# Optimization experiments

Hardware: AMD Instinct MI355X
Metric: run time of the kernel (lower is better)

## Reference

```python
import jax, jax.numpy as jnp
import numpy as np

N, E, H, ED, NF, NG = 75000, 150000, 44, 10, 15000, 1500


def _seg_mean(v, idx, n):
    s = jax.ops.segment_sum(v, idx, num_segments=n)
    c = jax.ops.segment_sum(jnp.ones((v.shape[0], 1), v.dtype), idx, num_segments=n)
    return s / jnp.maximum(c, 1.0)


def setup_inputs() -> dict:
    key = jax.random.key(0)
    ks = jax.random.split(key, 26)
    p = lambda k, shape: (jax.random.normal(k, shape, dtype=jnp.float32) * 0.1)
    x = jax.random.normal(ks[0], (N, H), dtype=jnp.float32)
    edge_index = jax.random.randint(ks[1], (2, E), 0, N)
    edge_attr = jax.random.normal(ks[2], (E, ED), dtype=jnp.float32)
    node2frag = (jnp.arange(N) * NF) // N          # sorted, covers all fragments
    frag2graph = (jnp.arange(NF) * NG) // NF       # sorted, covers all graphs
    noise = jax.random.normal(ks[3], (NF, H), dtype=jnp.float32)
    return {
        "x": x, "edge_attr": edge_attr, "noise": noise,
        "W0": p(ks[4], (H, H)), "b0": jnp.zeros((H,)),
        "We1": p(ks[5], (ED, ED)), "be1": jnp.zeros((ED,)),
        "We2": p(ks[6], (ED, H * H)), "be2": jnp.zeros((H * H,)),
        "root": p(ks[7], (H, H)), "conv_b": jnp.zeros((H,)),
        "Wm": p(ks[8], (2 * H, H)), "bm": jnp.zeros((H,)),
        "Wc1": p(ks[9], (H, H)), "bc1": jnp.zeros((H,)),
        "bn_g": jnp.ones((H,)), "bn_b": jnp.zeros((H,)),
        "Wc2": p(ks[10], (H, 1)), "bc2": jnp.zeros((1,)),
        "Wp1": p(ks[11], (H, 256)), "bp1": jnp.zeros((256,)),
        "Wp2": p(ks[12], (256, 128)), "bp2": jnp.zeros((128,)),
        "Wp3": p(ks[13], (128, 1)), "bp3": jnp.zeros((1,)),
        "edge_index": edge_index, "node2frag": node2frag, "frag2graph": frag2graph,
        "n_frags": NF, "n_graphs": NG,
    }


def reference(x, edge_attr, noise, W0, b0, We1, be1, We2, be2, root, conv_b, Wm, bm,
              Wc1, bc1, bn_g, bn_b, Wc2, bc2, Wp1, bp1, Wp2, bp2, Wp3, bp3,
              edge_index, node2frag, frag2graph, n_frags, n_graphs):
    n, h = x.shape
    init = x
    out = jax.nn.relu(x @ W0 + b0)
    # edge-conditioned weight matrices (computed once; edge_attr is fixed)
    ew = (jax.nn.relu(edge_attr @ We1 + be1) @ We2 + be2).reshape(-1, h, h)  # [E,h,h]
    src, dst = edge_index[0], edge_index[1]
    for _ in range(3):  # num_step_message_passing
        msg = jnp.einsum('eh,eho->eo', out[src], ew)               # per-edge matvec
        agg = jax.ops.segment_sum(msg, dst, num_segments=n)        # aggr='add'
        m = jax.nn.relu(agg + out @ root + conv_b)                 # NNConv + relu
        out = jnp.concatenate([m, out], axis=1) @ Wm + bm          # message_layer
    nodef = out + init
    # F.normalize(dim=1)
    nodef = nodef / jnp.maximum(jnp.linalg.norm(nodef, axis=1, keepdims=True), 1e-12)
    frag = _seg_mean(nodef, node2frag, n_frags)                    # global_mean_pool
    # compressor: Linear -> BatchNorm(train stats) -> ReLU -> Linear -> Sigmoid
    z = frag @ Wc1 + bc1
    z = (z - z.mean(0)) / jnp.sqrt(z.var(0) + 1e-5) * bn_g + bn_b
    w = jax.nn.sigmoid(jax.nn.relu(z) @ Wc2 + bc2).squeeze(-1)     # [NF]
    lp = w[:, None]
    ln = 1.0 - lp
    preserve_rate = (w > 0.5).astype(jnp.float32).mean()
    static = jax.lax.stop_gradient(frag)
    cnt = jax.ops.segment_sum(jnp.ones((n_frags,), jnp.float32), frag2graph, num_segments=n_graphs)[:, None]
    gsum = jax.ops.segment_sum(static, frag2graph, num_segments=n_graphs)
    gmean = gsum / jnp.maximum(cnt, 1.0)
    gsq = jax.ops.segment_sum(static * static, frag2graph, num_segments=n_graphs)
    gvar = (gsq - cnt * gmean * gmean) / jnp.maximum(cnt - 1.0, 1.0)  # unbiased (scatter_std)
    gstd = jnp.sqrt(jnp.maximum(gvar, 0.0))
    mean_f = gmean[frag2graph]
    std_f = gstd[frag2graph]
    nmean = lp * frag + ln * mean_f
    nstd = ln * std_f
    noisy = nmean + noise * nstd
    sub = _seg_mean(noisy, frag2graph, n_graphs)
    pred = jax.nn.sigmoid(jax.nn.relu(jax.nn.relu(sub @ Wp1 + bp1) @ Wp2 + bp2) @ Wp3 + bp3)
    eps = 1e-7
    kl = 0.5 * jax.ops.segment_sum((nstd ** 2 / (std_f + eps) ** 2).mean(axis=1), frag2graph, num_segments=n_graphs)[:, None] \
         + jax.ops.segment_sum(((nmean - mean_f) / (std_f + eps)) ** 2, frag2graph, num_segments=n_graphs)
    return pred, kl.mean(), preserve_rate
```

## Files before the change

### kernel.cpp

```cpp
#include <hip/hip_runtime.h>
#include <math.h>

#define NN 75000
#define NE 150000
#define H 44
#define HS 48
#define EDIM 10
#define NFRAG 15000
#define NGRAPH 1500

typedef const float* __restrict__ cfp;
typedef float* __restrict__ fpt;
typedef const int* __restrict__ cip;
typedef int* __restrict__ ipt;

__device__ __forceinline__ float relu_(float v){ return v>0.f?v:0.f; }
__device__ __forceinline__ float sigmoid_(float v){ return 1.f/(1.f+expf(-v)); }

__global__ __launch_bounds__(256) void k_hist(cip ei, ipt cnt){
    int e = blockIdx.x*256 + threadIdx.x;
    if(e>=NE) return;
    atomicAdd(&cnt[ei[NE+e]], 1);
}

__global__ __launch_bounds__(1024) void k_scan1(cip cnt, ipt incl, ipt bsum){
    __shared__ int sd[1024];
    int i = blockIdx.x*1024 + threadIdx.x;
    int v = (i<NN)? cnt[i] : 0;
    sd[threadIdx.x]=v;
    __syncthreads();
    for(int off=1; off<1024; off<<=1){
        int t = (threadIdx.x>=off)? sd[threadIdx.x-off] : 0;
        __syncthreads();
        sd[threadIdx.x]+=t;
        __syncthreads();
    }
    if(i<NN) incl[i]=sd[threadIdx.x];
    if(threadIdx.x==1023) bsum[blockIdx.x]=sd[1023];
}

__global__ void k_scan2(ipt bsum, int nblk){
    if(threadIdx.x==0 && blockIdx.x==0){
        int run=0;
        for(int b=0;b<nblk;b++){ int t=bsum[b]; bsum[b]=run; run+=t; }
    }
}

__global__ __launch_bounds__(1024) void k_scan3(cip incl, cip bsum, ipt rowptr){
    int i = blockIdx.x*1024 + threadIdx.x;
    if(i==0) rowptr[0]=0;
    if(i<NN) rowptr[i+1] = incl[i] + bsum[i>>10];
}

__global__ __launch_bounds__(256) void k_scatter(cip ei, cip rowptr, ipt cur, ipt eidx){
    int e = blockIdx.x*256 + threadIdx.x;
    if(e>=NE) return;
    int d = ei[NE+e];
    int pos = rowptr[d] + atomicAdd(&cur[d],1);
    eidx[pos]=e;
}

__global__ __launch_bounds__(256) void k_in(cfp x, cfp W0, cfp b0, fpt out){
    __shared__ float sW[H*H];
    __shared__ float sb[H];
    for(int i=threadIdx.x;i<H*H;i+=256) sW[i]=W0[i];
    if(threadIdx.x<H) sb[threadIdx.x]=b0[threadIdx.x];
    __syncthreads();
    int n = blockIdx.x*256 + threadIdx.x;
    if(n>=NN) return;
    float xv[H];
    const float4* xp = (const float4*)(x + (size_t)n*H);
    #pragma unroll
    for(int i=0;i<11;i++){ float4 v=xp[i]; xv[4*i]=v.x; xv[4*i+1]=v.y; xv[4*i+2]=v.z; xv[4*i+3]=v.w; }
    float acc[H];
    #pragma unroll
    for(int o=0;o<H;o++) acc[o]=sb[o];
    #pragma unroll
    for(int h=0;h<H;h++){
        float xh = xv[h];
        const float4* wr = (const float4*)(sW + h*H);
        #pragma unroll
        for(int o=0;o<11;o++){
            float4 w = wr[o];
            acc[4*o]+=xh*w.x; acc[4*o+1]+=xh*w.y; acc[4*o+2]+=xh*w.z; acc[4*o+3]+=xh*w.w;
        }
    }
    #pragma unroll
    for(int o=0;o<H;o++) acc[o]=relu_(acc[o]);
    float* row = out + (size_t)n*HS;
    #pragma unroll
    for(int s=0;s<4;s++){
        float4* p=(float4*)(row + s*12);
        p[0]=make_float4(acc[11*s+0],acc[11*s+1],acc[11*s+2],acc[11*s+3]);
        p[1]=make_float4(acc[11*s+4],acc[11*s+5],acc[11*s+6],acc[11*s+7]);
        p[2]=make_float4(acc[11*s+8],acc[11*s+9],acc[11*s+10],0.f);
    }
}

#define NB2 256
__global__ __launch_bounds__(256,3) void k_b2(cfp out, cfp be2, fpt b2){
    __shared__ float ovT[HS*NB2];
    int tid=threadIdx.x, lane=tid&63;
    int og = __builtin_amdgcn_readfirstlane(tid>>6);
    size_t base=(size_t)blockIdx.x*NB2;
    { size_t n=base+tid; size_t nc = n<NN? n : NN-1;
      const float4* orow=(const float4*)(out + nc*HS);
      #pragma unroll
      for(int i=0;i<12;i++){ float4 v=orow[i];
        ovT[(4*i+0)*NB2+tid]=v.x; ovT[(4*i+1)*NB2+tid]=v.y;
        ovT[(4*i+2)*NB2+tid]=v.z; ovT[(4*i+3)*NB2+tid]=v.w; }
    }
    __syncthreads();
    float m[4][11];
    #pragma unroll
    for(int j=0;j<4;j++)
        #pragma unroll
        for(int o=0;o<11;o++) m[j][o]=0.f;
    const float* wog = be2 + og*11;
    #pragma unroll
    for(int h=0;h<H;h++){
        int hl = h + h/11;
        const float4* ovp=(const float4*)(ovT + hl*NB2 + lane*4);
        float4 ov=ovp[0];
        #pragma unroll
        for(int o=0;o<11;o++){
            float w = wog[h*H+o];
            m[0][o]+=ov.x*w; m[1][o]+=ov.y*w; m[2][o]+=ov.z*w; m[3][o]+=ov.w*w;
        }
    }
    size_t n0 = base + (size_t)lane*4;
    #pragma unroll
    for(int j=0;j<4;j++){
        size_t n=n0+j;
        if(n<NN){
            float4* p=(float4*)(b2 + n*HS + og*12);
            p[0]=make_float4(m[j][0],m[j][1],m[j][2],m[j][3]);
            p[1]=make_float4(m[j][4],m[j][5],m[j][6],m[j][7]);
            p[2]=make_float4(m[j][8],m[j][9],m[j][10],0.f);
        }
    }
}

__global__ __launch_bounds__(256) void k_edge(cfp ea, cfp We1, cfp be1, fpt t){
    __shared__ float sW[EDIM*EDIM];
    __shared__ float sb[EDIM];
    if(threadIdx.x<EDIM*EDIM) sW[threadIdx.x]=We1[threadIdx.x];
    if(threadIdx.x<EDIM) sb[threadIdx.x]=be1[threadIdx.x];
    __syncthreads();
    int e = blockIdx.x*256 + threadIdx.x;
    if(e>=NE) return;
    float acc[EDIM];
    #pragma unroll
    for(int j=0;j<EDIM;j++) acc[j]=sb[j];
    #pragma unroll
    for(int k=0;k<EDIM;k++){
        float a = ea[(size_t)e*EDIM + k];
        #pragma unroll
        for(int j=0;j<EDIM;j++) acc[j]+=a*sW[k*EDIM+j];
    }
    #pragma unroll
    for(int j=0;j<EDIM;j++) t[(size_t)e*EDIM+j]=relu_(acc[j]);
}

#define EBM 256
__global__ __launch_bounds__(256,2) void k_msg(cfp out, cfp b2, cfp t, cfp We2, cip ei, fpt msg){
    __shared__ float ovT[HS*EBM];
    __shared__ float tT[EDIM*EBM];
    int tid=threadIdx.x, lane=tid&63;
    int og = __builtin_amdgcn_readfirstlane(tid>>6);
    size_t base=(size_t)blockIdx.x*EBM;
    { size_t e=base+tid; size_t ec = e<NE? e : NE-1;
      int s = ei[ec];
      const float4* orow=(const float4*)(out + (size_t)s*HS);
      #pragma unroll
      for(int i=0;i<12;i++){ float4 v=orow[i];
        ovT[(4*i+0)*EBM+tid]=v.x; ovT[(4*i+1)*EBM+tid]=v.y;
        ovT[(4*i+2)*EBM+tid]=v.z; ovT[(4*i+3)*EBM+tid]=v.w; }
      const float2* trow=(const float2*)(t + ec*EDIM);
      #pragma unroll
      for(int i=0;i<5;i++){ float2 v=trow[i]; tT[(2*i+0)*EBM+tid]=v.x; tT[(2*i+1)*EBM+tid]=v.y; }
    }
    __syncthreads();
    size_t e0 = base + (size_t)lane*4;
    int srcj[4];
    #pragma unroll
    for(int j=0;j<4;j++){ size_t e=e0+j; srcj[j]=ei[e<NE? e : NE-1]; }
    float m[4][11];
    #pragma unroll
    for(int j=0;j<4;j++){
        const float4* br=(const float4*)(b2 + (size_t)srcj[j]*HS + og*12);
        float4 A=br[0],B=br[1],C=br[2];
        m[j][0]=A.x; m[j][1]=A.y; m[j][2]=A.z; m[j][3]=A.w;
        m[j][4]=B.x; m[j][5]=B.y; m[j][6]=B.z; m[j][7]=B.w;
        m[j][8]=C.x; m[j][9]=C.y; m[j][10]=C.z;
    }
    const float* wog = We2 + og*11;
    for(int k=0;k<EDIM;k++){
        const float4* tp=(const float4*)(tT + k*EBM + lane*4);
        float4 t4=tp[0];
        const float* wk = wog + k*(H*H);
        #pragma unroll
        for(int h=0;h<H;h++){
            int hl = h + h/11;
            const float4* ovp=(const float4*)(ovT + hl*EBM + lane*4);
            float4 ov=ovp[0];
            float z0=t4.x*ov.x, z1=t4.y*ov.y, z2=t4.z*ov.z, z3=t4.w*ov.w;
            #pragma unroll
            for(int o=0;o<11;o++){
                float w = wk[h*H+o];
                m[0][o]+=z0*w; m[1][o]+=z1*w; m[2][o]+=z2*w; m[3][o]+=z3*w;
            }
        }
    }
    #pragma unroll
    for(int j=0;j<4;j++){
        size_t e=e0+j;
        if(e<NE){
            float4* p=(float4*)(msg + e*HS + og*12);
            p[0]=make_float4(m[j][0],m[j][1],m[j][2],m[j][3]);
            p[1]=make_float4(m[j][4],m[j][5],m[j][6],m[j][7]);
            p[2]=make_float4(m[j][8],m[j][9],m[j][10],0.f);
        }
    }
}

#define NBC 128
__global__ __launch_bounds__(256,3) void k_comb(cfp out, cfp msg, cip rowptr, cip eidx,
                                                cfp root, cfp conv_b, cfp Wm, cfp bm, fpt out_nxt){
    __shared__ float ovT[HS*NBC];
    __shared__ float mT[HS*NBC];
    int tid=threadIdx.x, lane=tid&63;
    int og = __builtin_amdgcn_readfirstlane(tid>>6);
    size_t base=(size_t)blockIdx.x*NBC;
    { int nl=tid>>1, half=tid&1;
      size_t n=base+nl; size_t nc = n<NN? n : NN-1;
      const float4* orow=(const float4*)(out + nc*HS + half*24);
      #pragma unroll
      for(int i=0;i<6;i++){ float4 v=orow[i];
        ovT[(half*24+4*i+0)*NBC+nl]=v.x; ovT[(half*24+4*i+1)*NBC+nl]=v.y;
        ovT[(half*24+4*i+2)*NBC+nl]=v.z; ovT[(half*24+4*i+3)*NBC+nl]=v.w; }
    }
    __syncthreads();
    size_t n0 = base + (size_t)lane*2;
    float m[2][11];
    #pragma unroll
    for(int j=0;j<2;j++)
        #pragma unroll
        for(int o=0;o<11;o++) m[j][o]=conv_b[og*11+o];
    #pragma unroll
    for(int j=0;j<2;j++){
        size_t n=n0+j; size_t nc = n<NN? n : NN-1;
        int st=rowptr[nc], en=rowptr[nc+1];
        for(int idx=st; idx<en; idx++){
            int e=eidx[idx];
            const float4* p=(const float4*)(msg + (size_t)e*HS + og*12);
            float4 A=p[0],B=p[1],C=p[2];
            m[j][0]+=A.x; m[j][1]+=A.y; m[j][2]+=A.z; m[j][3]+=A.w;
            m[j][4]+=B.x; m[j][5]+=B.y; m[j][6]+=B.z; m[j][7]+=B.w;
            m[j][8]+=C.x; m[j][9]+=C.y; m[j][10]+=C.z;
        }
    }
    const float* rog = root + og*11;
    #pragma unroll
    for(int h=0;h<H;h++){
        int hl = h + h/11;
        const float2* ovp=(const float2*)(ovT + hl*NBC + lane*2);
        float2 ov=ovp[0];
        #pragma unroll
        for(int o=0;o<11;o++){
            float w = rog[h*H+o];
            m[0][o]+=ov.x*w; m[1][o]+=ov.y*w;
        }
    }
    #pragma unroll
    for(int j=0;j<2;j++)
        #pragma unroll
        for(int o=0;o<11;o++) m[j][o]=relu_(m[j][o]);
    #pragma unroll
    for(int j=0;j<2;j++)
        #pragma unroll
        for(int o=0;o<11;o++) mT[(og*12+o)*NBC + lane*2+j]=m[j][o];
    __syncthreads();
    float no[2][11];
    #pragma unroll
    for(int j=0;j<2;j++)
        #pragma unroll
        for(int o=0;o<11;o++) no[j][o]=bm[og*11+o];
    const float* wmog = Wm + og*11;
    #pragma unroll
    for(int h=0;h<H;h++){
        int hl = h + h/11;
        const float2* mp=(const float2*)(mT + hl*NBC + lane*2);
        const float2* ovp=(const float2*)(ovT + hl*NBC + lane*2);
        float2 mh=mp[0], ov=ovp[0];
        #pragma unroll
        for(int o=0;o<11;o++){
            float a = wmog[h*H+o];
            float b = wmog[(H+h)*H+o];
            no[0][o]+=mh.x*a+ov.x*b;
            no[1][o]+=mh.y*a+ov.y*b;
        }
    }
    #pragma unroll
    for(int j=0;j<2;j++){
        size_t n=n0+j;
        if(n<NN){
            float4* p=(float4*)(out_nxt + n*HS + og*12);
            p[0]=make_float4(no[j][0],no[j][1],no[j][2],no[j][3]);
            p[1]=make_float4(no[j][4],no[j][5],no[j][6],no[j][7]);
            p[2]=make_float4(no[j][8],no[j][9],no[j][10],0.f);
        }
    }
}

__global__ __launch_bounds__(256,2) void k_frag(cfp out, cfp x, cfp Wc1, cfp bc1,
                                                fpt frag, fpt z, fpt colstat){
    __shared__ float nd[250*45];
    __shared__ float frS[50*45];
    __shared__ float sW[H*H];
    int tid=threadIdx.x;
    for(int i=tid;i<H*H;i+=256) sW[i]=Wc1[i];
    if(tid<250){
        int n = blockIdx.x*250 + tid;
        float v[H];
        const float4* xp=(const float4*)(x + (size_t)n*H);
        #pragma unroll
        for(int i=0;i<11;i++){ float4 a=xp[i]; v[4*i]=a.x; v[4*i+1]=a.y; v[4*i+2]=a.z; v[4*i+3]=a.w; }
        const float4* orow=(const float4*)(out + (size_t)n*HS);
        #pragma unroll
        for(int s=0;s<4;s++){
            float4 A=orow[3*s+0],B=orow[3*s+1],C=orow[3*s+2];
            v[11*s+0]+=A.x; v[11*s+1]+=A.y; v[11*s+2]+=A.z; v[11*s+3]+=A.w;
            v[11*s+4]+=B.x; v[11*s+5]+=B.y; v[11*s+6]+=B.z; v[11*s+7]+=B.w;
            v[11*s+8]+=C.x; v[11*s+9]+=C.y; v[11*s+10]+=C.z;
        }
        float ss=0.f;
        #pragma unroll
        for(int o=0;o<H;o++) ss+=v[o]*v[o];
        float inv = 1.f/fmaxf(sqrtf(ss),1e-12f);
        #pragma unroll
        for(int o=0;o<H;o++) nd[tid*45+o]=v[o]*inv;
    }
    __syncthreads();
    if(tid<50){
        float fr[H];
        #pragma unroll
        for(int o=0;o<H;o++) fr[o]=0.f;
        for(int j=0;j<5;j++){
            int r=tid*5+j;
            #pragma unroll
            for(int o=0;o<H;o++) fr[o]+=nd[r*45+o];
        }
        #pragma unroll
        for(int o=0;o<H;o++){ fr[o]*=0.2f; frS[tid*45+o]=fr[o]; }
        int f = blockIdx.x*50 + tid;
        float4* fw=(float4*)(frag + (size_t)f*H);
        #pragma unroll
        for(int i=0;i<11;i++) fw[i]=make_float4(fr[4*i],fr[4*i+1],fr[4*i+2],fr[4*i+3]);
    }
    __syncthreads();
    int fl=tid>>2, q=tid&3;
    int flc = fl<50? fl : 0;
    bool fv = fl<50;
    float zr[11];
    #pragma unroll
    for(int o=0;o<11;o++) zr[o]=bc1[q*11+o];
    for(int h=0;h<H;h++){
        float fh = frS[flc*45+h];
        #pragma unroll
        for(int o=0;o<11;o++) zr[o]+=fh*sW[h*H+q*11+o];
    }
    #pragma unroll
    for(int o=0;o<11;o++) if(!fv) zr[o]=0.f;
    if(fv){
        int f = blockIdx.x*50 + fl;
        #pragma unroll
        for(int o=0;o<11;o++) z[(size_t)f*H + q*11+o]=zr[o];
    }
    #pragma unroll
    for(int o=0;o<11;o++){
        float s=zr[o], sq=zr[o]*zr[o];
        #pragma unroll
        for(int d=4;d<64;d<<=1){ s+=__shfl_xor(s,d); sq+=__shfl_xor(sq,d); }
        if((tid&63)<4){
            atomicAdd(colstat + q*11+o, s);
            atomicAdd(colstat + H + q*11+o, sq);
        }
    }
}

__global__ __launch_bounds__(256) void k_bnw(cfp z, cfp colstat, cfp bng, cfp bnb, cfp Wc2, cfp bc2, fpt w, fpt pres){
    int f = blockIdx.x*256 + threadIdx.x;
    bool valid = f < NFRAG;
    int fc = valid ? f : NFRAG-1;
    float s = 0.f;
    #pragma unroll
    for(int o=0;o<H;o++){
        float mean = colstat[o]*(1.f/NFRAG);
        float var  = colstat[H+o]*(1.f/NFRAG) - mean*mean;
        float zb = (z[(size_t)fc*H+o]-mean)*rsqrtf(var+1e-5f)*bng[o]+bnb[o];
        s += relu_(zb)*Wc2[o];
    }
    float wv = sigmoid_(s + bc2[0]);
    if(valid) w[f]=wv;
    unsigned long long msk = __ballot(valid && (wv > 0.5f));
    if((threadIdx.x&63)==0) atomicAdd(pres,(float)__popcll(msk));
}

__global__ __launch_bounds__(64) void k_graph(cfp frag, cfp w, cfp noise, fpt sub, fpt klg){
    int g = blockIdx.x;
    int o = threadIdx.x;
    bool act = o < H;
    int oc = act ? o : 0;
    float frv[10];
    #pragma unroll
    for(int j=0;j<10;j++) frv[j] = act ? frag[(size_t)(10*g+j)*H + oc] : 0.f;
    float gs=0.f, gq=0.f;
    #pragma unroll
    for(int j=0;j<10;j++){ gs+=frv[j]; gq+=frv[j]*frv[j]; }
    float gmean = gs*0.1f;
    float gvar  = (gq - 10.f*gmean*gmean)*(1.f/9.f);
    float gstd  = sqrtf(fmaxf(gvar,0.f));
    float se    = gstd + 1e-7f;
    float c     = act ? (gstd/se)*(gstd/se) : 0.f;
    float C = c;
    #pragma unroll
    for(int dlt=32;dlt>0;dlt>>=1) C+=__shfl_xor(C,dlt);
    float subacc=0.f, B=0.f, Sln=0.f;
    #pragma unroll
    for(int j=0;j<10;j++){
        float lp = w[10*g+j];
        float ln = 1.f-lp;
        Sln += ln*ln;
        float nm = lp*frv[j] + ln*gmean;
        float ns = ln*gstd;
        float ny = nm + (act ? noise[(size_t)(10*g+j)*H + oc] : 0.f)*ns;
        subacc += ny;
        float dd = (nm-gmean)/se;
        B += dd*dd;
    }
    if(act) sub[(size_t)g*H+o] = subacc*0.1f;
    float Bv = act ? B : 0.f;
    #pragma unroll
    for(int dlt=32;dlt>0;dlt>>=1) Bv+=__shfl_xor(Bv,dlt);
    if(o==0) klg[g] = 0.5f*C*Sln + Bv;
}

__global__ __launch_bounds__(256) void k_pred(cfp sub, cfp Wp1, cfp bp1, cfp Wp2, cfp bp2,
                                              cfp Wp3, cfp bp3, fpt outp){
    __shared__ float ssub[H];
    __shared__ float sh1[256];
    __shared__ float sh2[128];
    int g = blockIdx.x; int tid = threadIdx.x;
    if(tid<H) ssub[tid] = sub[(size_t)g*H+tid];
    __syncthreads();
    float a = bp1[tid];
    for(int o=0;o<H;o++) a += ssub[o]*Wp1[(size_t)o*256+tid];
    sh1[tid]=relu_(a);
    __syncthreads();
    if(tid<128){
        float b = bp2[tid];
        for(int i=0;i<256;i++) b += sh1[i]*Wp2[(size_t)i*128+tid];
        sh2[tid]=relu_(b);
    }
    __syncthreads();
    if(tid<64){
        float s = sh2[tid]*Wp3[tid] + sh2[tid+64]*Wp3[tid+64];
        #pragma unroll
        for(int dlt=32;dlt>0;dlt>>=1) s+=__shfl_xor(s,dlt);
        if(tid==0) outp[g]=sigmoid_(s+bp3[0]);
    }
}

__global__ void k_final(cfp klg, cfp pres, fpt outp){
    float s = 0.f;
    for(int i=threadIdx.x;i<NGRAPH;i+=256) s+=klg[i];
    __shared__ float red[4];
    #pragma unroll
    for(int dlt=32;dlt>0;dlt>>=1) s+=__shfl_xor(s,dlt);
    int wid = threadIdx.x>>6;
    if((threadIdx.x&63)==0) red[wid]=s;
    __syncthreads();
    if(threadIdx.x==0){
        float tot = red[0]+red[1]+red[2]+red[3];
        outp[NGRAPH]   = tot/(float)(NGRAPH*H);
        outp[NGRAPH+1] = pres[0]/(float)NFRAG;
    }
}

extern "C" void kernel_launch(void* const* d_in, const int* in_sizes, int n_in,
                              void* d_out, int out_size, void* d_ws, size_t ws_size,
                              hipStream_t stream) {
    (void)in_sizes; (void)n_in; (void)out_size; (void)ws_size;
    const float* x        =(const float*)d_in[0];
    const float* edge_attr=(const float*)d_in[1];
    const float* noise    =(const float*)d_in[2];
    const float* W0       =(const float*)d_in[3];
    const float* b0       =(const float*)d_in[4];
    const float* We1      =(const float*)d_in[5];
    const float* be1      =(const float*)d_in[6];
    const float* We2      =(const float*)d_in[7];
    const float* be2      =(const float*)d_in[8];
    const float* root     =(const float*)d_in[9];
    const float* conv_b   =(const float*)d_in[10];
    const float* Wm       =(const float*)d_in[11];
    const float* bm       =(const float*)d_in[12];
    const float* Wc1      =(const float*)d_in[13];
    const float* bc1      =(const float*)d_in[14];
    const float* bng      =(const float*)d_in[15];
    const float* bnb      =(const float*)d_in[16];
    const float* Wc2      =(const float*)d_in[17];
    const float* bc2      =(const float*)d_in[18];
    const float* Wp1      =(const float*)d_in[19];
    const float* bp1      =(const float*)d_in[20];
    const float* Wp2      =(const float*)d_in[21];
    const float* bp2      =(const float*)d_in[22];
    const float* Wp3      =(const float*)d_in[23];
    const float* bp3      =(const float*)d_in[24];
    const int*   ei       =(const int*)d_in[25];

    float* ws = (float*)d_ws;
    const size_t NHS = (size_t)NN*HS;
    float* out_a  = ws;
    float* out_b  = out_a + NHS;
    float* b2_a   = out_b + NHS;
    float* b2_b   = b2_a + NHS;
    float* tbuf   = b2_b + NHS;
    float* msgbuf = tbuf + (size_t)NE*EDIM;
    float* frag   = msgbuf + (size_t)NE*HS;
    float* zbuf   = frag + (size_t)NFRAG*H;
    float* wv     = zbuf + (size_t)NFRAG*H;
    float* sub    = wv + NFRAG;
    float* klg    = sub + (size_t)NGRAPH*H;
    int*   rowptr = (int*)(klg + NGRAPH);
    int*   eidx   = rowptr + (NN+1);
    int*   bsum   = eidx + NE;
    int*   incl   = bsum + 128;
    int*   cnt    = incl + NN;
    int*   cur    = cnt + NN;
    float* colstat= (float*)(cur + NN);
    float* pres   = colstat + 2*H;

    hipMemsetAsync(cnt, 0, (size_t)(2*NN + 2*H + 8)*sizeof(float), stream);

    const int nb_n  = (NN + 255)/256;
    const int nb_e  = (NE + 255)/256;
    const int nb_f  = (NFRAG + 255)/256;
    const int nblk  = (NN + 1023)/1024;
    const int nb_c  = (NN + NBC-1)/NBC;

    k_hist   <<<nb_e,256,0,stream>>>(ei, cnt);
    k_scan1  <<<nblk,1024,0,stream>>>(cnt, incl, bsum);
    k_scan2  <<<1,64,0,stream>>>(bsum, nblk);
    k_scan3  <<<nblk,1024,0,stream>>>(incl, bsum, rowptr);
    k_scatter<<<nb_e,256,0,stream>>>(ei, rowptr, cur, eidx);

    k_in  <<<nb_n,256,0,stream>>>(x, W0, b0, out_a);
    k_b2  <<<nb_n,256,0,stream>>>(out_a, be2, b2_a);
    k_edge<<<nb_e,256,0,stream>>>(edge_attr, We1, be1, tbuf);

    float* cur_o = out_a; float* cur_b = b2_a;
    float* nxt_o = out_b; float* nxt_b = b2_b;
    for(int it=0; it<3; ++it){
        k_msg <<<nb_e,256,0,stream>>>(cur_o, cur_b, tbuf, We2, ei, msgbuf);
        k_comb<<<nb_c,256,0,stream>>>(cur_o, msgbuf, rowptr, eidx, root, conv_b, Wm, bm, nxt_o);
        if(it<2) k_b2<<<nb_n,256,0,stream>>>(nxt_o, be2, nxt_b);
        float* tp;
        tp=cur_o; cur_o=nxt_o; nxt_o=tp;
        tp=cur_b; cur_b=nxt_b; nxt_b=tp;
    }

    k_frag <<<300,256,0,stream>>>(cur_o, x, Wc1, bc1, frag, zbuf, colstat);
    k_bnw  <<<nb_f,256,0,stream>>>(zbuf, colstat, bng, bnb, Wc2, bc2, wv, pres);
    k_graph<<<NGRAPH,64,0,stream>>>(frag, wv, noise, sub, klg);
    k_pred <<<NGRAPH,256,0,stream>>>(sub, Wp1, bp1, Wp2, bp2, Wp3, bp3, (float*)d_out);
    k_final<<<1,256,0,stream>>>(klg, pres, (float*)d_out);
}
```

Measured before the change: 1.676 ms.

## Aggregate edge outer products per node before applying We2, dropping per-edge messages

Message passing is reordered algebraically. Each destination node first accumulates outer products of the edge features (plus a constant 1 for the be2 bias) with its source embeddings, using a sorted CSR with permuted source and edge-feature arrays. One per-node contraction against a padded We2/be2 tensor then replaces the per-edge 44x44 matrix products, the per-edge message buffer and the separate bias kernel. The combine kernel reads the aggregate directly and updates node states in place. BatchNorm column statistics now use per-block partials plus a reduction kernel instead of float atomics. The trade-off is higher register pressure in the new aggregation kernel and extra setup kernels, including a serial per-node insertion sort.

Measured after the change: 1.367 ms. -18.4%, faster.

```diff
diff --git a/kernel.cpp b/kernel.cpp
--- a/kernel.cpp
+++ b/kernel.cpp
@@ -60,6 +60,39 @@
     eidx[pos]=e;
 }
 
+__global__ __launch_bounds__(256) void k_sortcsr(cip rowptr, ipt eidx){
+    int n = blockIdx.x*256 + threadIdx.x;
+    if(n>=NN) return;
+    int st=rowptr[n], en=rowptr[n+1];
+    for(int i=st+1;i<en;i++){
+        int v=eidx[i]; int j=i-1;
+        while(j>=st && eidx[j]>v){ eidx[j+1]=eidx[j]; j--; }
+        eidx[j+1]=v;
+    }
+}
+
+__global__ __launch_bounds__(256) void k_perm(cip eidx, cip ei, cfp t, ipt srcP, fpt tP){
+    int p = blockIdx.x*256+threadIdx.x;
+    if(p>=NE) return;
+    int e = eidx[p];
+    srcP[p] = ei[e];
+    #pragma unroll
+    for(int k=0;k<EDIM;k++) tP[(size_t)p*12+k] = t[(size_t)e*EDIM+k];
+    tP[(size_t)p*12+10]=0.f; tP[(size_t)p*12+11]=0.f;
+}
+
+__global__ __launch_bounds__(256) void k_wprep(cfp We2, cfp be2, fpt WextP){
+    int idx = blockIdx.x*256 + threadIdx.x;
+    if(idx>=11*48*48) return;
+    int oo = idx%48, hh=(idx/48)%48, c=idx/(48*48);
+    float v=0.f;
+    if(oo%12!=11 && hh%12!=11){
+        int o = oo - oo/12, h = hh - hh/12;
+        v = (c<10)? We2[(size_t)c*1936 + h*44 + o] : be2[h*44+o];
+    }
+    WextP[idx]=v;
+}
+
 __global__ __launch_bounds__(256) void k_in(cfp x, cfp W0, cfp b0, fpt out){
     __shared__ float sW[H*H];
     __shared__ float sb[H];
@@ -97,50 +130,6 @@
     }
 }
 
-#define NB2 256
-__global__ __launch_bounds__(256,3) void k_b2(cfp out, cfp be2, fpt b2){
-    __shared__ float ovT[HS*NB2];
-    int tid=threadIdx.x, lane=tid&63;
-    int og = __builtin_amdgcn_readfirstlane(tid>>6);
-    size_t base=(size_t)blockIdx.x*NB2;
-    { size_t n=base+tid; size_t nc = n<NN? n : NN-1;
-      const float4* orow=(const float4*)(out + nc*HS);
-      #pragma unroll
-      for(int i=0;i<12;i++){ float4 v=orow[i];
-        ovT[(4*i+0)*NB2+tid]=v.x; ovT[(4*i+1)*NB2+tid]=v.y;
-        ovT[(4*i+2)*NB2+tid]=v.z; ovT[(4*i+3)*NB2+tid]=v.w; }
-    }
-    __syncthreads();
-    float m[4][11];
-    #pragma unroll
-    for(int j=0;j<4;j++)
-        #pragma unroll
-        for(int o=0;o<11;o++) m[j][o]=0.f;
-    const float* wog = be2 + og*11;
-    #pragma unroll
-    for(int h=0;h<H;h++){
-        int hl = h + h/11;
-        const float4* ovp=(const float4*)(ovT + hl*NB2 + lane*4);
-        float4 ov=ovp[0];
-        #pragma unroll
-        for(int o=0;o<11;o++){
-            float w = wog[h*H+o];
-            m[0][o]+=ov.x*w; m[1][o]+=ov.y*w; m[2][o]+=ov.z*w; m[3][o]+=ov.w*w;
-        }
-    }
-    size_t n0 = base + (size_t)lane*4;
-    #pragma unroll
-    for(int j=0;j<4;j++){
-        size_t n=n0+j;
-        if(n<NN){
-            float4* p=(float4*)(b2 + n*HS + og*12);
-            p[0]=make_float4(m[j][0],m[j][1],m[j][2],m[j][3]);
-            p[1]=make_float4(m[j][4],m[j][5],m[j][6],m[j][7]);
-            p[2]=make_float4(m[j][8],m[j][9],m[j][10],0.f);
-        }
-    }
-}
-
 __global__ __launch_bounds__(256) void k_edge(cfp ea, cfp We1, cfp be1, fpt t){
     __shared__ float sW[EDIM*EDIM];
     __shared__ float sb[EDIM];
@@ -162,71 +151,112 @@
     for(int j=0;j<EDIM;j++) t[(size_t)e*EDIM+j]=relu_(acc[j]);
 }
 
-#define EBM 256
-__global__ __launch_bounds__(256,2) void k_msg(cfp out, cfp b2, cfp t, cfp We2, cip ei, fpt msg){
-    __shared__ float ovT[HS*EBM];
-    __shared__ float tT[EDIM*EBM];
+__global__ __launch_bounds__(256,3) void k_Ragg(cfp out, cip rowptr, cip srcP, cfp tP, cfp WextP, fpt agg){
+    __shared__ float sP[4*44*64];
     int tid=threadIdx.x, lane=tid&63;
     int og = __builtin_amdgcn_readfirstlane(tid>>6);
-    size_t base=(size_t)blockIdx.x*EBM;
-    { size_t e=base+tid; size_t ec = e<NE? e : NE-1;
-      int s = ei[ec];
-      const float4* orow=(const float4*)(out + (size_t)s*HS);
-      #pragma unroll
-      for(int i=0;i<12;i++){ float4 v=orow[i];
-        ovT[(4*i+0)*EBM+tid]=v.x; ovT[(4*i+1)*EBM+tid]=v.y;
-        ovT[(4*i+2)*EBM+tid]=v.z; ovT[(4*i+3)*EBM+tid]=v.w; }
-      const float2* trow=(const float2*)(t + ec*EDIM);
-      #pragma unroll
-      for(int i=0;i<5;i++){ float2 v=trow[i]; tT[(2*i+0)*EBM+tid]=v.x; tT[(2*i+1)*EBM+tid]=v.y; }
-    }
-    __syncthreads();
-    size_t e0 = base + (size_t)lane*4;
-    int srcj[4];
-    #pragma unroll
-    for(int j=0;j<4;j++){ size_t e=e0+j; srcj[j]=ei[e<NE? e : NE-1]; }
-    float m[4][11];
-    #pragma unroll
-    for(int j=0;j<4;j++){
-        const float4* br=(const float4*)(b2 + (size_t)srcj[j]*HS + og*12);
-        float4 A=br[0],B=br[1],C=br[2];
-        m[j][0]=A.x; m[j][1]=A.y; m[j][2]=A.z; m[j][3]=A.w;
-        m[j][4]=B.x; m[j][5]=B.y; m[j][6]=B.z; m[j][7]=B.w;
-        m[j][8]=C.x; m[j][9]=C.y; m[j][10]=C.z;
-    }
-    const float* wog = We2 + og*11;
-    for(int k=0;k<EDIM;k++){
-        const float4* tp=(const float4*)(tT + k*EBM + lane*4);
-        float4 t4=tp[0];
-        const float* wk = wog + k*(H*H);
-        #pragma unroll
-        for(int h=0;h<H;h++){
-            int hl = h + h/11;
-            const float4* ovp=(const float4*)(ovT + hl*EBM + lane*4);
-            float4 ov=ovp[0];
-            float z0=t4.x*ov.x, z1=t4.y*ov.y, z2=t4.z*ov.z, z3=t4.w*ov.w;
-            #pragma unroll
-            for(int o=0;o<11;o++){
-                float w = wk[h*H+o];
-                m[0][o]+=z0*w; m[1][o]+=z1*w; m[2][o]+=z2*w; m[3][o]+=z3*w;
+    int n = blockIdx.x*64 + lane;
+    int st=0, en=0;
+    if(n<NN){ st=rowptr[n]; en=rowptr[n+1]; }
+    float P[44];
+    #pragma unroll
+    for(int o=0;o<44;o++) P[o]=0.f;
+
+    {
+        float acc[6][11];
+        #pragma unroll
+        for(int c=0;c<6;c++)
+            #pragma unroll
+            for(int i=0;i<11;i++) acc[c][i]=0.f;
+        for(int j=st;j<en;j++){
+            int s = srcP[j];
+            const float4* tp4=(const float4*)(tP + (size_t)j*12);
+            float4 ta=tp4[0];
+            float2 tb2=*(const float2*)(tP + (size_t)j*12 + 4);
+            float tk[6] = {ta.x,ta.y,ta.z,ta.w, tb2.x,tb2.y};
+            const float4* ov4=(const float4*)(out + (size_t)s*HS + og*12);
+            float4 oa=ov4[0], ob=ov4[1], oc=ov4[2];
+            float ovv[11] = {oa.x,oa.y,oa.z,oa.w, ob.x,ob.y,ob.z,ob.w, oc.x,oc.y,oc.z};
+            #pragma unroll
+            for(int c=0;c<6;c++)
+                #pragma unroll
+                for(int i=0;i<11;i++) acc[c][i]+=tk[c]*ovv[i];
+        }
+        #pragma unroll
+        for(int c=0;c<6;c++){
+            #pragma unroll
+            for(int i=0;i<11;i++){
+                float a = acc[c][i];
+                const float4* wr=(const float4*)(WextP + ((size_t)c*48 + og*12 + i)*48);
+                #pragma unroll
+                for(int q=0;q<4;q++){
+                    float4 wA=wr[3*q], wB=wr[3*q+1], wC=wr[3*q+2];
+                    P[q*11+0]+=a*wA.x; P[q*11+1]+=a*wA.y; P[q*11+2]+=a*wA.z; P[q*11+3]+=a*wA.w;
+                    P[q*11+4]+=a*wB.x; P[q*11+5]+=a*wB.y; P[q*11+6]+=a*wB.z; P[q*11+7]+=a*wB.w;
+                    P[q*11+8]+=a*wC.x; P[q*11+9]+=a*wC.y; P[q*11+10]+=a*wC.z;
+                }
             }
         }
     }
-    #pragma unroll
-    for(int j=0;j<4;j++){
-        size_t e=e0+j;
-        if(e<NE){
-            float4* p=(float4*)(msg + e*HS + og*12);
-            p[0]=make_float4(m[j][0],m[j][1],m[j][2],m[j][3]);
-            p[1]=make_float4(m[j][4],m[j][5],m[j][6],m[j][7]);
-            p[2]=make_float4(m[j][8],m[j][9],m[j][10],0.f);
-        }
+    {
+        float acc[5][11];
+        #pragma unroll
+        for(int c=0;c<5;c++)
+            #pragma unroll
+            for(int i=0;i<11;i++) acc[c][i]=0.f;
+        for(int j=st;j<en;j++){
+            int s = srcP[j];
+            const float4* tp4=(const float4*)(tP + (size_t)j*12 + 4);
+            float4 tb=tp4[0];
+            float2 tc2=*(const float2*)(tP + (size_t)j*12 + 8);
+            float tk[4] = {tb.z,tb.w, tc2.x,tc2.y};
+            const float4* ov4=(const float4*)(out + (size_t)s*HS + og*12);
+            float4 oa=ov4[0], ob=ov4[1], oc=ov4[2];
+            float ovv[11] = {oa.x,oa.y,oa.z,oa.w, ob.x,ob.y,ob.z,ob.w, oc.x,oc.y,oc.z};
+            #pragma unroll
+            for(int c=0;c<4;c++)
+                #pragma unroll
+                for(int i=0;i<11;i++) acc[c][i]+=tk[c]*ovv[i];
+            #pragma unroll
+            for(int i=0;i<11;i++) acc[4][i]+=ovv[i];
+        }
+        #pragma unroll
+        for(int c=0;c<5;c++){
+            #pragma unroll
+            for(int i=0;i<11;i++){
+                float a = acc[c][i];
+                const float4* wr=(const float4*)(WextP + ((size_t)(c+6)*48 + og*12 + i)*48);
+                #pragma unroll
+                for(int q=0;q<4;q++){
+                    float4 wA=wr[3*q], wB=wr[3*q+1], wC=wr[3*q+2];
+                    P[q*11+0]+=a*wA.x; P[q*11+1]+=a*wA.y; P[q*11+2]+=a*wA.z; P[q*11+3]+=a*wA.w;
+                    P[q*11+4]+=a*wB.x; P[q*11+5]+=a*wB.y; P[q*11+6]+=a*wB.z; P[q*11+7]+=a*wB.w;
+                    P[q*11+8]+=a*wC.x; P[q*11+9]+=a*wC.y; P[q*11+10]+=a*wC.z;
+                }
+            }
+        }
+    }
+    #pragma unroll
+    for(int o=0;o<44;o++) sP[((size_t)og*44+o)*64 + lane] = P[o];
+    __syncthreads();
+    float m[11];
+    #pragma unroll
+    for(int i=0;i<11;i++){
+        int o = og*11+i;
+        m[i] = sP[(0*44+o)*64+lane] + sP[(1*44+o)*64+lane]
+             + sP[(2*44+o)*64+lane] + sP[(3*44+o)*64+lane];
+    }
+    if(n<NN){
+        float4* p=(float4*)(agg + (size_t)n*HS + og*12);
+        p[0]=make_float4(m[0],m[1],m[2],m[3]);
+        p[1]=make_float4(m[4],m[5],m[6],m[7]);
+        p[2]=make_float4(m[8],m[9],m[10],0.f);
     }
 }
 
 #define NBC 128
-__global__ __launch_bounds__(256,3) void k_comb(cfp out, cfp msg, cip rowptr, cip eidx,
-                                                cfp root, cfp conv_b, cfp Wm, cfp bm, fpt out_nxt){
+__global__ __launch_bounds__(256,3) void k_comb(fpt out, cfp agg,
+                                                cfp root, cfp conv_b, cfp Wm, cfp bm){
     __shared__ float ovT[HS*NBC];
     __shared__ float mT[HS*NBC];
     int tid=threadIdx.x, lane=tid&63;
@@ -244,21 +274,15 @@
     size_t n0 = base + (size_t)lane*2;
     float m[2][11];
     #pragma unroll
-    for(int j=0;j<2;j++)
-        #pragma unroll
-        for(int o=0;o<11;o++) m[j][o]=conv_b[og*11+o];
-    #pragma unroll
     for(int j=0;j<2;j++){
         size_t n=n0+j; size_t nc = n<NN? n : NN-1;
-        int st=rowptr[nc], en=rowptr[nc+1];
-        for(int idx=st; idx<en; idx++){
-            int e=eidx[idx];
-            const float4* p=(const float4*)(msg + (size_t)e*HS + og*12);
-            float4 A=p[0],B=p[1],C=p[2];
-            m[j][0]+=A.x; m[j][1]+=A.y; m[j][2]+=A.z; m[j][3]+=A.w;
-            m[j][4]+=B.x; m[j][5]+=B.y; m[j][6]+=B.z; m[j][7]+=B.w;
-            m[j][8]+=C.x; m[j][9]+=C.y; m[j][10]+=C.z;
-        }
+        const float4* ap=(const float4*)(agg + nc*HS + og*12);
+        float4 A=ap[0],B=ap[1],C=ap[2];
+        m[j][0]=A.x; m[j][1]=A.y; m[j][2]=A.z; m[j][3]=A.w;
+        m[j][4]=B.x; m[j][5]=B.y; m[j][6]=B.z; m[j][7]=B.w;
+        m[j][8]=C.x; m[j][9]=C.y; m[j][10]=C.z;
+        #pragma unroll
+        for(int o=0;o<11;o++) m[j][o]+=conv_b[og*11+o];
     }
     const float* rog = root + og*11;
     #pragma unroll
@@ -305,7 +329,7 @@
     for(int j=0;j<2;j++){
         size_t n=n0+j;
         if(n<NN){
-            float4* p=(float4*)(out_nxt + n*HS + og*12);
+            float4* p=(float4*)(out + n*HS + og*12);
             p[0]=make_float4(no[j][0],no[j][1],no[j][2],no[j][3]);
             p[1]=make_float4(no[j][4],no[j][5],no[j][6],no[j][7]);
             p[2]=make_float4(no[j][8],no[j][9],no[j][10],0.f);
@@ -314,10 +338,11 @@
 }
 
 __global__ __launch_bounds__(256,2) void k_frag(cfp out, cfp x, cfp Wc1, cfp bc1,
-                                                fpt frag, fpt z, fpt colstat){
+                                                fpt frag, fpt z, fpt colpart){
     __shared__ float nd[250*45];
     __shared__ float frS[50*45];
     __shared__ float sW[H*H];
+    __shared__ float sP[4*176];
     int tid=threadIdx.x;
     for(int i=tid;i<H*H;i+=256) sW[i]=Wc1[i];
     if(tid<250){
@@ -377,16 +402,32 @@
         #pragma unroll
         for(int o=0;o<11;o++) z[(size_t)f*H + q*11+o]=zr[o];
     }
+    int wid = tid>>6;
     #pragma unroll
     for(int o=0;o<11;o++){
         float s=zr[o], sq=zr[o]*zr[o];
         #pragma unroll
         for(int d=4;d<64;d<<=1){ s+=__shfl_xor(s,d); sq+=__shfl_xor(sq,d); }
         if((tid&63)<4){
-            atomicAdd(colstat + q*11+o, s);
-            atomicAdd(colstat + H + q*11+o, sq);
-        }
-    }
+            sP[wid*176 + q*11+o] = s;
+            sP[wid*176 + 88 + q*11+o] = sq;
+        }
+    }
+    __syncthreads();
+    if(tid<176){
+        float s = sP[tid] + sP[176+tid] + sP[352+tid] + sP[528+tid];
+        colpart[(size_t)blockIdx.x*176 + tid] = s;
+    }
+}
+
+__global__ __launch_bounds__(64) void k_colred(cfp colpart, fpt colstat){
+    int col = blockIdx.x;
+    int tid = threadIdx.x;
+    float s = 0.f;
+    for(int b=tid;b<300;b+=64) s += colpart[(size_t)b*176 + col];
+    #pragma unroll
+    for(int d=32;d>0;d>>=1) s+=__shfl_xor(s,d);
+    if(tid==0) colstat[col]=s;
 }
 
 __global__ __launch_bounds__(256) void k_bnw(cfp z, cfp colstat, cfp bng, cfp bnb, cfp Wc2, cfp bc2, fpt w, fpt pres){
@@ -522,57 +563,56 @@
     float* ws = (float*)d_ws;
     const size_t NHS = (size_t)NN*HS;
     float* out_a  = ws;
-    float* out_b  = out_a + NHS;
-    float* b2_a   = out_b + NHS;
-    float* b2_b   = b2_a + NHS;
-    float* tbuf   = b2_b + NHS;
-    float* msgbuf = tbuf + (size_t)NE*EDIM;
-    float* frag   = msgbuf + (size_t)NE*HS;
+    float* agg    = out_a + NHS;
+    float* tbuf   = agg + NHS;
+    float* tP     = tbuf + (size_t)NE*EDIM;
+    float* frag   = tP + (size_t)NE*12;
     float* zbuf   = frag + (size_t)NFRAG*H;
     float* wv     = zbuf + (size_t)NFRAG*H;
     float* sub    = wv + NFRAG;
     float* klg    = sub + (size_t)NGRAPH*H;
-    int*   rowptr = (int*)(klg + NGRAPH);
+    float* WextP  = klg + NGRAPH;
+    float* colpart= WextP + 11*48*48;
+    float* colstat= colpart + 300*176;
+    int*   rowptr = (int*)(colstat + 176 + 16);
     int*   eidx   = rowptr + (NN+1);
-    int*   bsum   = eidx + NE;
+    int*   srcP   = eidx + NE;
+    int*   bsum   = srcP + NE;
     int*   incl   = bsum + 128;
     int*   cnt    = incl + NN;
     int*   cur    = cnt + NN;
-    float* colstat= (float*)(cur + NN);
-    float* pres   = colstat + 2*H;
-
-    hipMemsetAsync(cnt, 0, (size_t)(2*NN + 2*H + 8)*sizeof(float), stream);
+    float* pres   = (float*)(cur + NN);
+
+    hipMemsetAsync(cnt, 0, (size_t)(2*NN)*sizeof(int) + 4*sizeof(float), stream);
 
     const int nb_n  = (NN + 255)/256;
     const int nb_e  = (NE + 255)/256;
     const int nb_f  = (NFRAG + 255)/256;
     const int nblk  = (NN + 1023)/1024;
     const int nb_c  = (NN + NBC-1)/NBC;
+    const int nb_r  = (NN + 63)/64;
 
     k_hist   <<<nb_e,256,0,stream>>>(ei, cnt);
     k_scan1  <<<nblk,1024,0,stream>>>(cnt, incl, bsum);
     k_scan2  <<<1,64,0,stream>>>(bsum, nblk);
     k_scan3  <<<nblk,1024,0,stream>>>(incl, bsum, rowptr);
     k_scatter<<<nb_e,256,0,stream>>>(ei, rowptr, cur, eidx);
-
-    k_in  <<<nb_n,256,0,stream>>>(x, W0, b0, out_a);
-    k_b2  <<<nb_n,256,0,stream>>>(out_a, be2, b2_a);
-    k_edge<<<nb_e,256,0,stream>>>(edge_attr, We1, be1, tbuf);
-
-    float* cur_o = out_a; float* cur_b = b2_a;
-    float* nxt_o = out_b; float* nxt_b = b2_b;
+    k_sortcsr<<<nb_n,256,0,stream>>>(rowptr, eidx);
+
+    k_edge <<<nb_e,256,0,stream>>>(edge_attr, We1, be1, tbuf);
+    k_perm <<<nb_e,256,0,stream>>>(eidx, ei, tbuf, srcP, tP);
+    k_wprep<<<(11*48*48+255)/256,256,0,stream>>>(We2, be2, WextP);
+    k_in   <<<nb_n,256,0,stream>>>(x, W0, b0, out_a);
+
     for(int it=0; it<3; ++it){
-        k_msg <<<nb_e,256,0,stream>>>(cur_o, cur_b, tbuf, We2, ei, msgbuf);
-        k_comb<<<nb_c,256,0,stream>>>(cur_o, msgbuf, rowptr, eidx, root, conv_b, Wm, bm, nxt_o);
-        if(it<2) k_b2<<<nb_n,256,0,stream>>>(nxt_o, be2, nxt_b);
-        float* tp;
-        tp=cur_o; cur_o=nxt_o; nxt_o=tp;
-        tp=cur_b; cur_b=nxt_b; nxt_b=tp;
-    }
-
-    k_frag <<<300,256,0,stream>>>(cur_o, x, Wc1, bc1, frag, zbuf, colstat);
-    k_bnw  <<<nb_f,256,0,stream>>>(zbuf, colstat, bng, bnb, Wc2, bc2, wv, pres);
-    k_graph<<<NGRAPH,64,0,stream>>>(frag, wv, noise, sub, klg);
-    k_pred <<<NGRAPH,256,0,stream>>>(sub, Wp1, bp1, Wp2, bp2, Wp3, bp3, (float*)d_out);
-    k_final<<<1,256,0,stream>>>(klg, pres, (float*)d_out);
-}
+        k_Ragg<<<nb_r,256,0,stream>>>(out_a, rowptr, srcP, tP, WextP, agg);
+        k_comb<<<nb_c,256,0,stream>>>(out_a, agg, root, conv_b, Wm, bm);
+    }
+
+    k_frag  <<<300,256,0,stream>>>(out_a, x, Wc1, bc1, frag, zbuf, colpart);
+    k_colred<<<176,64,0,stream>>>(colpart, colstat);
+    k_bnw   <<<nb_f,256,0,stream>>>(zbuf, colstat, bng, bnb, Wc2, bc2, wv, pres);
+    k_graph <<<NGRAPH,64,0,stream>>>(frag, wv, noise, sub, klg);
+    k_pred  <<<NGRAPH,256,0,stream>>>(sub, Wp1, bp1, Wp2, bp2, Wp3, bp3, (float*)d_out);
+    k_final <<<1,256,0,stream>>>(klg, pres, (float*)d_out);
+}
```
